# Kernel optimization log

Measured on AMD Instinct MI355X. Metric: run time of the kernel, lower is better.

Reference implementation:

```python
import jax, jax.numpy as jnp
import numpy as np

B, C, H, W = 16, 256, 56, 56
HEADS = 4
C_OUT = 256
K = 3
SQ = 16  # squeeze_rate (C=256 >= 80, so not halved)
BN_EPS = 1e-5


def setup_inputs() -> dict:
    key = jax.random.key(0)
    ks = jax.random.split(key, 9)
    r = C // SQ
    cper = C_OUT // HEADS
    return {
        "x": jax.random.normal(ks[0], (B, C, H, W), dtype=jnp.float32),
        "bn_gamma": 1.0 + 0.1 * jax.random.normal(ks[1], (C,), dtype=jnp.float32),
        "bn_beta": 0.1 * jax.random.normal(ks[2], (C,), dtype=jnp.float32),
        "bn_mean": 0.1 * jax.random.normal(ks[3], (C,), dtype=jnp.float32),
        "bn_var": 0.5 + jax.random.uniform(ks[4], (C,), dtype=jnp.float32),
        "fc1_w": 0.1 * jax.random.normal(ks[5], (HEADS, r, C), dtype=jnp.float32),
        "fc2_w": 0.1 * jax.random.normal(ks[6], (HEADS, C, r), dtype=jnp.float32),
        "fc2_b": jnp.ones((HEADS, C), dtype=jnp.float32),  # init.constant_(bias, 1.0)
        "conv_w": 0.05 * jax.random.normal(ks[7], (HEADS, cper, C, K, K), dtype=jnp.float32),
        "inactive_channels": 192,
    }


def reference(x, bn_gamma, bn_beta, bn_mean, bn_var, fc1_w, fc2_w, fc2_b, conv_w, inactive_channels):
    b, c, h, w = x.shape
    heads = fc1_w.shape[0]
    # BatchNorm (inference, running stats) + ReLU
    inv = jax.lax.rsqrt(bn_var + BN_EPS)
    xn = jax.nn.relu((x - bn_mean[None, :, None, None]) * (bn_gamma * inv)[None, :, None, None]
                     + bn_beta[None, :, None, None])
    # Global average pool -> [b, c]
    x_avg = xn.mean(axis=(2, 3))
    # Per-head SE gate: relu(fc2(relu(fc1(x_avg))))  -> [heads, b, c]
    y1 = jax.nn.relu(jnp.einsum("bc,hrc->hbr", x_avg, fc1_w))
    mask = jax.nn.relu(jnp.einsum("hbr,hcr->hbc", y1, fc2_w) + fc2_b[:, None, :])
    lasso_loss = mask.mean(axis=(1, 2)).sum()  # sum over heads of per-head mean
    # topk smallest -> threshold; zero out mask values <= k-th smallest (detached cmp)
    mask_d = jax.lax.stop_gradient(mask)
    if inactive_channels > 0:
        neg_vals, _ = jax.lax.top_k(-mask_d, inactive_channels)  # k largest of -mask
        thresh = -neg_vals[..., -1:]  # k-th smallest of mask, [heads, b, 1]
        mask_c = jnp.where(mask_d <= thresh, 0.0, mask)
    else:
        mask_c = mask
    # Apply per-head channel mask and stack heads: [b, heads*c, h, w]
    mc = jnp.transpose(mask_c, (1, 0, 2))  # [b, heads, c]
    x_mask = (xn[:, None, :, :, :] * mc[:, :, :, None, None]).reshape(b, heads * c, h, w)
    # Grouped conv (groups=heads), weight [heads*cper, c, K, K]
    wflat = conv_w.reshape(-1, c, K, K)
    out = jax.lax.conv_general_dilated(
        x_mask, wflat, window_strides=(1, 1), padding=[(1, 1), (1, 1)],
        dimension_numbers=("NCHW", "OIHW", "NCHW"), feature_group_count=heads)
    bo, co, ho, wo = out.shape
    out = out.reshape(bo, heads, co // heads, ho, wo).transpose(0, 2, 1, 3, 4).reshape(bo, co, ho, wo)
    return out, lasso_loss
```

## Files before the change

### kernel.cpp

```cpp
#include <hip/hip_runtime.h>
#include <hip/hip_bf16.h>
#include <math.h>

#define B_     16
#define C_     256
#define H_     56
#define W_     56
#define HEADS_ 4
#define CPER_  64
#define R_     16
#define HW_    (H_*W_)
#define BN_EPS_ 1e-5f

typedef short bf16x8 __attribute__((ext_vector_type(8)));
typedef float f32x4  __attribute__((ext_vector_type(4)));

__device__ inline unsigned short f2bf(float f) {
    unsigned int u = __builtin_bit_cast(unsigned int, f);
    u += 0x7fffu + ((u >> 16) & 1u);
    return (unsigned short)(u >> 16);
}

__global__ __launch_bounds__(64) void k_pool(
    const float* __restrict__ x,
    const float* __restrict__ gamma, const float* __restrict__ beta,
    const float* __restrict__ mean,  const float* __restrict__ var,
    float* __restrict__ xavg)
{
    int plane = blockIdx.x;
    int c = plane & (C_ - 1);
    float s = gamma[c] * rsqrtf(var[c] + BN_EPS_);
    float t = fmaf(-mean[c], s, beta[c]);
    const float4* xp = (const float4*)(x + (size_t)plane * HW_);
    float sum = 0.f;
    for (int i = threadIdx.x; i < HW_ / 4; i += 64) {
        float4 v = xp[i];
        sum += fmaxf(fmaf(v.x, s, t), 0.f) + fmaxf(fmaf(v.y, s, t), 0.f)
             + fmaxf(fmaf(v.z, s, t), 0.f) + fmaxf(fmaf(v.w, s, t), 0.f);
    }
    for (int off = 32; off; off >>= 1) sum += __shfl_down(sum, off, 64);
    if (threadIdx.x == 0) xavg[plane] = sum * (1.f / HW_);
}

__global__ __launch_bounds__(256) void k_wt2(const float* __restrict__ w,
                                             float* __restrict__ wt2f)
{
    int i = blockIdx.x * 256 + threadIdx.x;
    if (i >= HEADS_ * 9 * CPER_ * C_) return;
    int c = i & 255, j = (i >> 8) & 63, ht = i >> 14;
    int h = ht / 9, t = ht - h * 9;
    wt2f[i] = w[((size_t)((h * CPER_ + j) * C_ + c)) * 9 + t];
}

__global__ __launch_bounds__(256) void k_se(
    const float* __restrict__ xavg,
    const float* __restrict__ fc1, const float* __restrict__ fc2,
    const float* __restrict__ fc2b, const int* __restrict__ kptr,
    float* __restrict__ maskc, int* __restrict__ aidx64,
    int* __restrict__ act_cnt, float* __restrict__ lasso)
{
    int hb = blockIdx.x;
    int h = hb / B_, b = hb - h * B_;
    int tid = threadIdx.x;

    __shared__ float sav[C_], sy1[R_], smask[C_], sred[4], sthr;
    __shared__ int scnt, s_ord[C_];

    sav[tid] = xavg[b * C_ + tid];
    if (tid == 0) scnt = 0;
    __syncthreads();

    if (tid < R_) {
        const float* w = fc1 + (size_t)(h * R_ + tid) * C_;
        float acc = 0.f;
        for (int c2 = 0; c2 < C_; ++c2) acc = fmaf(sav[c2], w[c2], acc);
        sy1[tid] = fmaxf(acc, 0.f);
    }
    __syncthreads();

    const float* w2 = fc2 + (size_t)(h * C_ + tid) * R_;
    float acc = fc2b[h * C_ + tid];
    for (int r = 0; r < R_; ++r) acc = fmaf(sy1[r], w2[r], acc);
    float m = fmaxf(acc, 0.f);
    smask[tid] = m;
    __syncthreads();

    float ls = m;
    for (int off = 32; off > 0; off >>= 1) ls += __shfl_down(ls, off, 64);
    int lane = tid & 63, wv = tid >> 6;
    if (lane == 0) sred[wv] = ls;

    int cl = 0, ce = 0;
    for (int j = 0; j < C_; ++j) {
        float vj = smask[j];
        cl += (vj < m);
        ce += (vj == m);
    }
    if (tid == 0) sthr = -1e30f;
    __syncthreads();
    int k = kptr[0];
    if (k > 0 && cl <= k - 1 && (k - 1) < cl + ce) sthr = m;
    __syncthreads();

    float thr = sthr;
    float mc = (m <= thr) ? 0.f : m;
    maskc[hb * C_ + tid] = mc;
    if (mc != 0.f) {
        int p = atomicAdd(&scnt, 1);
        s_ord[p] = tid;
    }
    __syncthreads();
    if (tid < 64) aidx64[hb * 64 + tid] = (tid < scnt) ? s_ord[tid] : 0;
    if (tid == 0) {
        act_cnt[hb] = scnt;
        atomicAdd(lasso, (sred[0] + sred[1] + sred[2] + sred[3]) * (1.f / (B_ * C_)));
    }
}

__global__ __launch_bounds__(256) void k_wgather(
    const float* __restrict__ wt2f, const float* __restrict__ maskc,
    const int* __restrict__ aidx64, const int* __restrict__ acnt,
    short* __restrict__ Wc)
{
    int t = blockIdx.x, hb = blockIdx.y;
    int h = hb >> 4;
    int tid = threadIdx.x;
    int cnt = acnt[hb];
    __shared__ int s_act[64];
    __shared__ float s_mv[64];
    if (tid < 64) {
        int a = aidx64[hb * 64 + tid];
        s_act[tid] = a;
        s_mv[tid]  = (tid < cnt) ? maskc[hb * C_ + a] : 0.f;
    }
    __syncthreads();
    const float* wsrc = wt2f + (size_t)(h * 9 + t) * (CPER_ * C_);
    short* wdst = Wc + (size_t)(hb * 9 + t) * (CPER_ * 64);
    for (int it = 0; it < 16; ++it) {
        int e = it * 256 + tid;
        int cp = e & 63, j = e >> 6;
        float v = wsrc[j * C_ + s_act[cp]] * s_mv[cp];
        int slot = (cp + 8 * (j & 7)) & 63;
        wdst[j * 64 + slot] = (short)f2bf(v);
    }
}

__global__ __launch_bounds__(256) void k_bnc(
    const float* __restrict__ x,
    const float* __restrict__ gamma, const float* __restrict__ beta,
    const float* __restrict__ mean,  const float* __restrict__ var,
    const int* __restrict__ aidx64, short* __restrict__ xc)
{
    int y = blockIdx.x, b = blockIdx.y;
    int tid = threadIdx.x;
    int h = tid >> 6;
    __shared__ __align__(16) unsigned short T[W_ * 256];

    int c = aidx64[(h * B_ + b) * 64 + (tid & 63)];
    float s = gamma[c] * rsqrtf(var[c] + BN_EPS_);
    float t0 = fmaf(-mean[c], s, beta[c]);
    const float* xrow = x + ((size_t)(b * C_ + c)) * HW_ + y * W_;
    #pragma unroll
    for (int f = 0; f < 14; ++f) {
        float4 v = *(const float4*)(xrow + f * 4);
        int px = f * 4;
        T[(px + 0) * 256 + tid] = f2bf(fmaxf(fmaf(v.x, s, t0), 0.f));
        T[(px + 1) * 256 + tid] = f2bf(fmaxf(fmaf(v.y, s, t0), 0.f));
        T[(px + 2) * 256 + tid] = f2bf(fmaxf(fmaf(v.z, s, t0), 0.f));
        T[(px + 3) * 256 + tid] = f2bf(fmaxf(fmaf(v.w, s, t0), 0.f));
    }
    __syncthreads();

    const uint2* Ts = (const uint2*)T;
    uint2* ob = (uint2*)xc;
    #pragma unroll
    for (int it = 0; it < 14; ++it) {
        int e = it * 256 + tid;
        int px = e >> 6, col4 = e & 63;
        int hh = col4 >> 4, cp4 = col4 & 15;
        uint2 v = Ts[px * 64 + col4];
        ob[((size_t)(hh * B_ + b) * HW_ + (size_t)y * W_ + px) * 16 + cp4] = v;
    }
}

__global__ __launch_bounds__(256, 4) void k_conv(
    const short* __restrict__ xc, const short* __restrict__ Wc,
    float* __restrict__ out)
{
    int g = blockIdx.x;
    int vx = g & 7, r = g >> 3;
    int hb = vx * 8 + r / 14;
    int band = r - (r / 14) * 14;
    int h = hb >> 4, b = hb & 15;
    int tid = threadIdx.x, lane = tid & 63, wv = tid >> 6;
    int y0 = band * 4;
    int m = lane & 15, q = lane >> 4;

    __shared__ short sW[5 * 4096];

    const short* Wh = Wc + (size_t)hb * 9 * 4096;
    const short* xb = xc + (size_t)hb * HW_ * 64;

    #pragma unroll
    for (int it = 0; it < 10; ++it) {
        int e = it * 256 + tid;
        *(bf16x8*)&sW[e * 8] = *(const bf16x8*)(Wh + e * 8);
    }
    __syncthreads();

    f32x4 acc[4][4];
    #pragma unroll
    for (int i = 0; i < 4; ++i)
        #pragma unroll
        for (int j = 0; j < 4; ++j)
            #pragma unroll
            for (int rr = 0; rr < 4; ++rr) acc[i][j][rr] = 0.f;

    int yrow = y0 + wv;
    int arot = q * 8 + 8 * (m & 7);

    #pragma unroll
    for (int t = 0; t < 9; ++t) {
        if (t == 5) {
            __syncthreads();
            #pragma unroll
            for (int it = 0; it < 8; ++it) {
                int e = it * 256 + tid;
                *(bf16x8*)&sW[e * 8] = *(const bf16x8*)(Wh + 20480 + e * 8);
            }
            __syncthreads();
        }
        const int dy = t / 3 - 1, dx = t % 3 - 1;
        int gy = yrow + dy;
        bool gyok = (unsigned)gy < (unsigned)H_;
        const short* sWc = sW + (t < 5 ? t : t - 5) * 4096;

        #pragma unroll
        for (int c0 = 0; c0 < 64; c0 += 32) {
            bf16x8 aF[4], bF[4];
            #pragma unroll
            for (int jt = 0; jt < 4; ++jt)
                aF[jt] = *(const bf16x8*)&sWc[(jt * 16 + m) * 64 + ((c0 + arot) & 63)];
            #pragma unroll
            for (int xt = 0; xt < 4; ++xt) {
                int gx = xt * 16 + m + dx;
                bf16x8 v = {0, 0, 0, 0, 0, 0, 0, 0};
                if (gyok && (unsigned)gx < (unsigned)W_)
                    v = *(const bf16x8*)(xb + ((size_t)(gy * W_ + gx)) * 64 + c0 + q * 8);
                bF[xt] = v;
            }
            __builtin_amdgcn_s_setprio(1);
            #pragma unroll
            for (int jt = 0; jt < 4; ++jt)
                #pragma unroll
                for (int xt = 0; xt < 4; ++xt)
                    acc[jt][xt] = __builtin_amdgcn_mfma_f32_16x16x32_bf16(
                        aF[jt], bF[xt], acc[jt][xt], 0, 0, 0);
            __builtin_amdgcn_s_setprio(0);
        }
    }

    #pragma unroll
    for (int xt = 0; xt < 4; ++xt) {
        int xx = xt * 16 + m;
        if (xx < W_) {
            #pragma unroll
            for (int jt = 0; jt < 4; ++jt)
                #pragma unroll
                for (int rr = 0; rr < 4; ++rr) {
                    int j = jt * 16 + q * 4 + rr;
                    int oc = j * HEADS_ + h;
                    out[(((size_t)b * C_ + oc) * H_ + yrow) * W_ + xx] = acc[jt][xt][rr];
                }
        }
    }
}

extern "C" void kernel_launch(void* const* d_in, const int* in_sizes, int n_in,
                              void* d_out, int out_size, void* d_ws, size_t ws_size,
                              hipStream_t stream)
{
    const float* x     = (const float*)d_in[0];
    const float* gamma = (const float*)d_in[1];
    const float* beta  = (const float*)d_in[2];
    const float* mean  = (const float*)d_in[3];
    const float* var   = (const float*)d_in[4];
    const float* fc1   = (const float*)d_in[5];
    const float* fc2   = (const float*)d_in[6];
    const float* fc2b  = (const float*)d_in[7];
    const float* convw = (const float*)d_in[8];
    const int*   kptr  = (const int*)d_in[9];

    float* out   = (float*)d_out;
    float* lasso = out + (size_t)B_ * C_ * HW_;

    char* ws = (char*)d_ws;
    size_t off = 0;
    short* xc    = (short*)(ws + off); off += (size_t)HEADS_ * B_ * HW_ * 64 * 2;
    off = (off + 255) & ~(size_t)255;
    float* xavg  = (float*)(ws + off); off += (size_t)B_ * C_ * 4;
    float* maskc = (float*)(ws + off); off += (size_t)HEADS_ * B_ * C_ * 4;
    int*   aidx64= (int*)  (ws + off); off += (size_t)HEADS_ * B_ * 64 * 4;
    int*   acnt  = (int*)  (ws + off); off += (size_t)HEADS_ * B_ * 4;
    off = (off + 255) & ~(size_t)255;
    float* wt2f  = (float*)(ws + off); off += (size_t)HEADS_ * 9 * CPER_ * C_ * 4;
    off = (off + 255) & ~(size_t)255;
    short* Wc    = (short*)(ws + off); off += (size_t)HEADS_ * B_ * 9 * CPER_ * 64 * 2;

    hipMemsetAsync(lasso, 0, 4, stream);

    k_wt2<<<(HEADS_ * 9 * CPER_ * C_ + 255) / 256, 256, 0, stream>>>(convw, wt2f);
    k_pool<<<B_ * C_, 64, 0, stream>>>(x, gamma, beta, mean, var, xavg);
    k_se<<<HEADS_ * B_, 256, 0, stream>>>(xavg, fc1, fc2, fc2b, kptr,
                                          maskc, aidx64, acnt, lasso);
    k_wgather<<<dim3(9, HEADS_ * B_), 256, 0, stream>>>(wt2f, maskc, aidx64, acnt, Wc);
    k_bnc<<<dim3(H_, B_), 256, 0, stream>>>(x, gamma, beta, mean, var, aidx64, xc);
    k_conv<<<HEADS_ * B_ * (H_ / 4), 256, 0, stream>>>(xc, Wc, out);
}
```

Measured before the change: 191.8 us.

## Drop weight transpose kernel and read conv weights directly from global memory

Removes the k_wt2 transpose pre-pass, so k_wgather gathers directly from the original strided conv weight layout. It also drops the LDS staging of weights in k_conv: A fragments are now loaded straight from global/L2 with an unswizzled layout, and the two block-wide barriers go away. Launch bounds are relaxed from 4 to 3 blocks per CU. The trade-off is that the weight gather becomes strided (stride 9) and the conv reloads weights per wave from cache instead of from shared memory, with possibly lower occupancy.

```diff
diff --git a/kernel.cpp b/kernel.cpp
--- a/kernel.cpp
+++ b/kernel.cpp
@@ -42,16 +42,6 @@
     if (threadIdx.x == 0) xavg[plane] = sum * (1.f / HW_);
 }
 
-__global__ __launch_bounds__(256) void k_wt2(const float* __restrict__ w,
-                                             float* __restrict__ wt2f)
-{
-    int i = blockIdx.x * 256 + threadIdx.x;
-    if (i >= HEADS_ * 9 * CPER_ * C_) return;
-    int c = i & 255, j = (i >> 8) & 63, ht = i >> 14;
-    int h = ht / 9, t = ht - h * 9;
-    wt2f[i] = w[((size_t)((h * CPER_ + j) * C_ + c)) * 9 + t];
-}
-
 __global__ __launch_bounds__(256) void k_se(
     const float* __restrict__ xavg,
     const float* __restrict__ fc1, const float* __restrict__ fc2,
@@ -118,7 +108,7 @@
 }
 
 __global__ __launch_bounds__(256) void k_wgather(
-    const float* __restrict__ wt2f, const float* __restrict__ maskc,
+    const float* __restrict__ convw, const float* __restrict__ maskc,
     const int* __restrict__ aidx64, const int* __restrict__ acnt,
     short* __restrict__ Wc)
 {
@@ -134,14 +124,13 @@
         s_mv[tid]  = (tid < cnt) ? maskc[hb * C_ + a] : 0.f;
     }
     __syncthreads();
-    const float* wsrc = wt2f + (size_t)(h * 9 + t) * (CPER_ * C_);
+    const float* wsrc = convw + (size_t)h * CPER_ * C_ * 9;
     short* wdst = Wc + (size_t)(hb * 9 + t) * (CPER_ * 64);
     for (int it = 0; it < 16; ++it) {
         int e = it * 256 + tid;
         int cp = e & 63, j = e >> 6;
-        float v = wsrc[j * C_ + s_act[cp]] * s_mv[cp];
-        int slot = (cp + 8 * (j & 7)) & 63;
-        wdst[j * 64 + slot] = (short)f2bf(v);
+        float v = wsrc[((size_t)j * C_ + s_act[cp]) * 9 + t] * s_mv[cp];
+        wdst[j * 64 + cp] = (short)f2bf(v);
     }
 }
 
@@ -183,7 +172,7 @@
     }
 }
 
-__global__ __launch_bounds__(256, 4) void k_conv(
+__global__ __launch_bounds__(256, 3) void k_conv(
     const short* __restrict__ xc, const short* __restrict__ Wc,
     float* __restrict__ out)
 {
@@ -193,20 +182,11 @@
     int band = r - (r / 14) * 14;
     int h = hb >> 4, b = hb & 15;
     int tid = threadIdx.x, lane = tid & 63, wv = tid >> 6;
-    int y0 = band * 4;
     int m = lane & 15, q = lane >> 4;
-
-    __shared__ short sW[5 * 4096];
+    int yrow = band * 4 + wv;
 
     const short* Wh = Wc + (size_t)hb * 9 * 4096;
     const short* xb = xc + (size_t)hb * HW_ * 64;
-
-    #pragma unroll
-    for (int it = 0; it < 10; ++it) {
-        int e = it * 256 + tid;
-        *(bf16x8*)&sW[e * 8] = *(const bf16x8*)(Wh + e * 8);
-    }
-    __syncthreads();
 
     f32x4 acc[4][4];
     #pragma unroll
@@ -216,31 +196,19 @@
             #pragma unroll
             for (int rr = 0; rr < 4; ++rr) acc[i][j][rr] = 0.f;
 
-    int yrow = y0 + wv;
-    int arot = q * 8 + 8 * (m & 7);
-
     #pragma unroll
     for (int t = 0; t < 9; ++t) {
-        if (t == 5) {
-            __syncthreads();
-            #pragma unroll
-            for (int it = 0; it < 8; ++it) {
-                int e = it * 256 + tid;
-                *(bf16x8*)&sW[e * 8] = *(const bf16x8*)(Wh + 20480 + e * 8);
-            }
-            __syncthreads();
-        }
         const int dy = t / 3 - 1, dx = t % 3 - 1;
         int gy = yrow + dy;
         bool gyok = (unsigned)gy < (unsigned)H_;
-        const short* sWc = sW + (t < 5 ? t : t - 5) * 4096;
+        const short* Wt = Wh + t * 4096;
 
         #pragma unroll
         for (int c0 = 0; c0 < 64; c0 += 32) {
             bf16x8 aF[4], bF[4];
             #pragma unroll
             for (int jt = 0; jt < 4; ++jt)
-                aF[jt] = *(const bf16x8*)&sWc[(jt * 16 + m) * 64 + ((c0 + arot) & 63)];
+                aF[jt] = *(const bf16x8*)(Wt + (jt * 16 + m) * 64 + c0 + q * 8);
             #pragma unroll
             for (int xt = 0; xt < 4; ++xt) {
                 int gx = xt * 16 + m + dx;
@@ -303,17 +271,14 @@
     int*   aidx64= (int*)  (ws + off); off += (size_t)HEADS_ * B_ * 64 * 4;
     int*   acnt  = (int*)  (ws + off); off += (size_t)HEADS_ * B_ * 4;
     off = (off + 255) & ~(size_t)255;
-    float* wt2f  = (float*)(ws + off); off += (size_t)HEADS_ * 9 * CPER_ * C_ * 4;
-    off = (off + 255) & ~(size_t)255;
     short* Wc    = (short*)(ws + off); off += (size_t)HEADS_ * B_ * 9 * CPER_ * 64 * 2;
 
     hipMemsetAsync(lasso, 0, 4, stream);
 
-    k_wt2<<<(HEADS_ * 9 * CPER_ * C_ + 255) / 256, 256, 0, stream>>>(convw, wt2f);
     k_pool<<<B_ * C_, 64, 0, stream>>>(x, gamma, beta, mean, var, xavg);
     k_se<<<HEADS_ * B_, 256, 0, stream>>>(xavg, fc1, fc2, fc2b, kptr,
                                           maskc, aidx64, acnt, lasso);
-    k_wgather<<<dim3(9, HEADS_ * B_), 256, 0, stream>>>(wt2f, maskc, aidx64, acnt, Wc);
+    k_wgather<<<dim3(9, HEADS_ * B_), 256, 0, stream>>>(convw, maskc, aidx64, acnt, Wc);
     k_bnc<<<dim3(H_, B_), 256, 0, stream>>>(x, gamma, beta, mean, var, aidx64, xc);
     k_conv<<<HEADS_ * B_ * (H_ / 4), 256, 0, stream>>>(xc, Wc, out);
 }
```

Measured after the change: 223.5 us. 1.17x slower.
